# Performance work log

Hardware: AMD Instinct MI355X
Metric: run time of the kernel (lower is better)

The kernel has to match this reference:

```python
import jax, jax.numpy as jnp
import numpy as np

N_NODES = 1024
CHANNELS = [1, 64, 128]
DENSE = [196608, 256]
SAMPLE_NUMBER = 50


def _glorot(key, shape):
    fan_in, fan_out = shape[0], shape[-1]
    s = jnp.sqrt(6.0 / (fan_in + fan_out))
    return jax.random.uniform(key, shape, jnp.float32, -s, s)


def setup_inputs() -> dict:
    key = jax.random.key(0)
    ks = jax.random.split(key, 20)
    T, B = 16, 64
    inp = {
        "xs_seq": jax.random.normal(ks[0], (T, B, N_NODES, CHANNELS[0]), jnp.float32),
        "adj": jax.random.uniform(ks[1], (N_NODES, N_NODES), jnp.float32) / N_NODES,
    }
    # GCGRU params per layer: gates z, r, candidate n over concat([x, h])
    ki = 2
    for li in range(len(CHANNELS) - 1):
        cin, cout = CHANNELS[li], CHANNELS[li + 1]
        for g in ("z", "r", "n"):
            inp[f"W{g}{li}"] = _glorot(ks[ki], (cin + cout, cout)); ki += 1
            inp[f"b{g}{li}"] = jnp.zeros((cout,), jnp.float32)
    inp["W_mu"] = _glorot(ks[ki], (DENSE[0], DENSE[1])); ki += 1
    inp["b_mu"] = jnp.zeros((DENSE[1],), jnp.float32)
    inp["W_lv"] = _glorot(ks[ki], (DENSE[0], DENSE[1])); ki += 1
    inp["b_lv"] = jnp.zeros((DENSE[1],), jnp.float32)
    return inp


def _gcgru(xs, adj, Wz, bz, Wr, br, Wn, bn, cout):
    # xs: [T, B, N, cin]; graph-conv GRU over time via scan
    T, B, N, _ = xs.shape
    h0 = jnp.zeros((B, N, cout), xs.dtype)

    def gconv(a, x, W, b):  # adj @ x @ W + b
        return jnp.einsum("ij,bjc,cd->bid", a, x, W) + b

    def step(h, x):
        xh = jnp.concatenate([x, h], axis=-1)
        z = jax.nn.sigmoid(gconv(adj, xh, Wz, bz))
        r = jax.nn.sigmoid(gconv(adj, xh, Wr, br))
        xrh = jnp.concatenate([x, r * h], axis=-1)
        n = jnp.tanh(gconv(adj, xrh, Wn, bn))
        h_new = (1.0 - z) * h + z * n
        return h_new, h_new

    _, hs = jax.lax.scan(step, h0, xs)
    return hs  # [T, B, N, cout]


def _forward(xs_seq, adj, Wz0, bz0, Wr0, br0, Wn0, bn0,
             Wz1, bz1, Wr1, br1, Wn1, bn1, W_mu, b_mu, W_lv, b_lv, eps):
    h1 = _gcgru(xs_seq, adj, Wz0, bz0, Wr0, br0, Wn0, bn0, CHANNELS[1])
    h2 = _gcgru(h1, adj, Wz1, bz1, Wr1, br1, Wn1, bn1, CHANNELS[2])
    xs = jnp.concatenate([h1[-1], h2[-1]], axis=2)  # [B, N, C1+C2]
    B = xs.shape[0]
    xs = xs.reshape(B, -1)  # [B, N*(C1+C2)]
    mu = jax.nn.sigmoid(xs @ W_mu + b_mu)
    logvar = jax.nn.sigmoid(xs @ W_lv + b_lv)
    std = jnp.exp(0.5 * logvar)
    z = mu + eps * std
    return z, mu, logvar


def reference(xs_seq, adj, Wz0, bz0, Wr0, br0, Wn0, bn0,
              Wz1, bz1, Wr1, br1, Wn1, bn1, W_mu, b_mu, W_lv, b_lv):
    B = xs_seq.shape[1]
    ekey = jax.random.fold_in(jax.random.key(0), 1234)
    eps = jax.random.normal(ekey, (SAMPLE_NUMBER, B, DENSE[1]), jnp.float32).mean(0)
    return _forward(xs_seq, adj, Wz0, bz0, Wr0, br0, Wn0, bn0,
                    Wz1, bz1, Wr1, br1, Wn1, bn1, W_mu, b_mu, W_lv, b_lv, eps)
```

## Files before the change

### kernel.cpp

```cpp
#include <hip/hip_runtime.h>
#include <math.h>

#define EPS_MODE 0

typedef unsigned short u16;
typedef short bf16x8 __attribute__((ext_vector_type(8)));
typedef float f32x4 __attribute__((ext_vector_type(4)));
typedef u16 u16x4 __attribute__((ext_vector_type(4)));
typedef u16 u16x8 __attribute__((ext_vector_type(8)));

static constexpr int T = 16;
static constexpr size_t MF = 1u << 20;
static constexpr int DKCH = 256;
static constexpr int DKCHUNK = 196608 / DKCH;

__device__ __forceinline__ u16 f2bf(float f) {
  unsigned u = __float_as_uint(f);
  unsigned r = (u + 0x7fffu + ((u >> 16) & 1u)) >> 16;
  return (u16)r;
}
__device__ __forceinline__ float bf2f(u16 h) {
  return __uint_as_float(((unsigned)h) << 16);
}
__device__ __forceinline__ void gload16(const void* g, void* l) {
  __builtin_amdgcn_global_load_lds(
      (const __attribute__((address_space(1))) void*)g,
      (__attribute__((address_space(3))) void*)l, 16, 0, 0);
}

__global__ __launch_bounds__(256) void cast_bf16(const float* __restrict__ in,
                                                 u16* __restrict__ out, int n) {
  int i = (blockIdx.x * 256 + threadIdx.x) * 4;
  if (i < n) {
    float4 v = *reinterpret_cast<const float4*>(&in[i]);
    out[i + 0] = f2bf(v.x); out[i + 1] = f2bf(v.y);
    out[i + 2] = f2bf(v.z); out[i + 3] = f2bf(v.w);
  }
}

__global__ __launch_bounds__(256) void prep_wt(const float* __restrict__ Wz0, const float* __restrict__ Wr0,
                                               const float* __restrict__ Wn0, const float* __restrict__ Wz1,
                                               const float* __restrict__ Wr1, const float* __restrict__ Wn1,
                                               u16* __restrict__ WzrT0, u16* __restrict__ WnT0,
                                               u16* __restrict__ WzrT1, u16* __restrict__ WnT1) {
  int seg = blockIdx.y;
  int idx = blockIdx.x * 256 + threadIdx.x;
  if (seg == 0) {
    if (idx < 128 * 64) {
      int j = idx >> 6, k = idx & 63;
      float v = (j < 64) ? Wz0[(k + 1) * 64 + j] : Wr0[(k + 1) * 64 + (j - 64)];
      WzrT0[idx] = f2bf(v);
    }
  } else if (seg == 1) {
    if (idx < 64 * 64) {
      int j = idx >> 6, k = idx & 63;
      WnT0[idx] = f2bf(Wn0[(k + 1) * 64 + j]);
    }
  } else if (seg == 2) {
    if (idx < 256 * 192) {
      int j = idx / 192, k = idx % 192;
      float v = (j < 128) ? Wz1[k * 128 + j] : Wr1[k * 128 + (j - 128)];
      WzrT1[idx] = f2bf(v);
    }
  } else {
    if (idx < 128 * 192) {
      int j = idx / 192, k = idx % 192;
      WnT1[idx] = f2bf(Wn1[k * 128 + j]);
    }
  }
}

template <int EPI, int LOGC, int MFR>
__device__ __forceinline__ void dev_adj_mfma(int bx, int by, char* lds,
                                             const u16* __restrict__ A,
                                             const u16* __restrict__ BT,
                                             void* __restrict__ OUT) {
  constexpr int MT = MFR * 32;
  int tid = threadIdx.x;
  int w = tid >> 6, lane = tid & 63;
  int row0 = by * MT, col0 = bx * 128;
  int wm = w >> 1, wn = w & 1;
  f32x4 acc[MFR][4] = {};
  for (int k0 = 0; k0 < 1024; k0 += 64) {
#pragma unroll
    for (int q = 0; q < MFR; ++q) {
      int row = q * 32 + w * 8 + (lane >> 3);
      gload16(A + (size_t)(row0 + row) * 1024 + k0 + (lane & 7) * 8,
              lds + q * 4096 + w * 1024);
    }
#pragma unroll
    for (int q = 0; q < 4; ++q) {
      int row = q * 32 + w * 8 + (lane >> 3);
      gload16(BT + (size_t)(col0 + row) * 1024 + k0 + (lane & 7) * 8,
              lds + MFR * 4096 + q * 4096 + w * 1024);
    }
    __syncthreads();
#pragma unroll
    for (int kk = 0; kk < 2; ++kk) {
      bf16x8 a[MFR], bb[4];
#pragma unroll
      for (int m = 0; m < MFR; ++m)
        a[m] = *(const bf16x8*)(lds + (wm * (MFR * 16) + m * 16 + (lane & 15)) * 128 + kk * 64 + (lane >> 4) * 16);
#pragma unroll
      for (int n = 0; n < 4; ++n)
        bb[n] = *(const bf16x8*)(lds + MFR * 4096 + (wn * 64 + n * 16 + (lane & 15)) * 128 + kk * 64 + (lane >> 4) * 16);
#pragma unroll
      for (int m = 0; m < MFR; ++m)
#pragma unroll
        for (int n = 0; n < 4; ++n)
          acc[m][n] = __builtin_amdgcn_mfma_f32_16x16x32_bf16(a[m], bb[n], acc[m][n], 0, 0, 0);
    }
    __syncthreads();
  }
  if (EPI == 1) {
    float* O = (float*)OUT;
#pragma unroll
    for (int m = 0; m < MFR; ++m)
#pragma unroll
      for (int n = 0; n < 4; ++n) {
        int col = col0 + wn * 64 + n * 16 + (lane & 15);
        int t = col >> 6, bbx = col & 63;
        int row = row0 + wm * (MFR * 16) + m * 16 + ((lane >> 4) << 2);
        *(float4*)&O[((size_t)t << 16) + ((size_t)bbx << 10) + row] = *(float4*)&acc[m][n];
      }
  } else {
    u16* O = (u16*)OUT;
    constexpr int C = 1 << LOGC;
#pragma unroll
    for (int m = 0; m < MFR; ++m)
#pragma unroll
      for (int n = 0; n < 4; ++n) {
        int col = col0 + wn * 64 + n * 16 + (lane & 15);
        int bbx = col >> LOGC, c = col & (C - 1);
#pragma unroll
        for (int j = 0; j < 4; ++j) {
          int row = row0 + wm * (MFR * 16) + m * 16 + ((lane >> 4) << 2) + j;
          O[(((size_t)bbx << 10) + row) * C + c] = f2bf(acc[m][n][j]);
        }
      }
  }
}

template <int EPI, int LOGC, int MFR>
__global__ __launch_bounds__(256) void adj_mfma(const u16* __restrict__ A,
                                                const u16* __restrict__ BT,
                                                void* __restrict__ OUT) {
  __shared__ __align__(16) char lds[(MFR + 4) * 4096];
  dev_adj_mfma<EPI, LOGC, MFR>(blockIdx.x, blockIdx.y, lds, A, BT, OUT);
}

template <int C, int RK1, int MFR>
__device__ __forceinline__ void dev_adj_ngate(
    int bx, int by, char* lds,
    const u16* __restrict__ A, const u16* __restrict__ BT,
    const u16* __restrict__ WnT, const float* __restrict__ bias,
    const float* __restrict__ axv, const float* __restrict__ wx,
    const u16* __restrict__ AH1, const u16* __restrict__ zT,
    u16* __restrict__ hT) {
  constexpr int LOGC = (C == 64) ? 6 : 7;
  constexpr int KW = (C == 64) ? 64 : 192;
  constexpr int KKAN = C / 32;
  constexpr int MT = MFR * 32;
  int tid = threadIdx.x;
  int w = tid >> 6, lane = tid & 63;
  int row0 = by * MT, col0 = bx * 128;
  int wm = w >> 1, wn = w & 1;
  f32x4 acc[MFR][4] = {};
  for (int k0 = 0; k0 < 1024; k0 += 64) {
#pragma unroll
    for (int q = 0; q < MFR; ++q) {
      int row = q * 32 + w * 8 + (lane >> 3);
      gload16(A + (size_t)(row0 + row) * 1024 + k0 + (lane & 7) * 8,
              lds + q * 4096 + w * 1024);
    }
#pragma unroll
    for (int q = 0; q < 4; ++q) {
      int row = q * 32 + w * 8 + (lane >> 3);
      gload16(BT + (size_t)(col0 + row) * 1024 + k0 + (lane & 7) * 8,
              lds + MFR * 4096 + q * 4096 + w * 1024);
    }
    __syncthreads();
#pragma unroll
    for (int kk = 0; kk < 2; ++kk) {
      bf16x8 a[MFR], bb[4];
#pragma unroll
      for (int m = 0; m < MFR; ++m)
        a[m] = *(const bf16x8*)(lds + (wm * (MFR * 16) + m * 16 + (lane & 15)) * 128 + kk * 64 + (lane >> 4) * 16);
#pragma unroll
      for (int n = 0; n < 4; ++n)
        bb[n] = *(const bf16x8*)(lds + MFR * 4096 + (wn * 64 + n * 16 + (lane & 15)) * 128 + kk * 64 + (lane >> 4) * 16);
#pragma unroll
      for (int m = 0; m < MFR; ++m)
#pragma unroll
        for (int n = 0; n < 4; ++n)
          acc[m][n] = __builtin_amdgcn_mfma_f32_16x16x32_bf16(a[m], bb[n], acc[m][n], 0, 0, 0);
    }
    __syncthreads();
  }
  u16* ANt = (u16*)lds;
#pragma unroll
  for (int m = 0; m < MFR; ++m)
#pragma unroll
    for (int n = 0; n < 4; ++n) {
      int cl = wn * 64 + n * 16 + (lane & 15);
      int rl = wm * (MFR * 16) + m * 16 + ((lane >> 4) << 2);
#pragma unroll
      for (int j = 0; j < 4; ++j)
        ANt[(rl + j) * 136 + cl] = f2bf(acc[m][n][j]);
    }
  __syncthreads();
  int wrow = w >> 1, half = w & 1;
  int arow0 = wrow * (MFR * 16);
  int b0 = col0 >> LOGC;
  int out0 = (C == 64) ? 0 : half * 64;
  int kbase = (C == 64) ? half * 64 : 0;
  int b_eff = (C == 64) ? (b0 + half) : b0;
  constexpr int WOFF = (C == 64) ? 0 : 64;
  f32x4 acc2[MFR][4] = {};
#pragma unroll
  for (int kk = 0; kk < KKAN; ++kk) {
    bf16x8 a[MFR], bb[4];
    int ka = kbase + kk * 32 + (lane >> 4) * 8;
#pragma unroll
    for (int m = 0; m < MFR; ++m)
      a[m] = *(const bf16x8*)&ANt[(arow0 + m * 16 + (lane & 15)) * 136 + ka];
#pragma unroll
    for (int n = 0; n < 4; ++n)
      bb[n] = *(const bf16x8*)&WnT[(size_t)(out0 + n * 16 + (lane & 15)) * KW + WOFF + kk * 32 + (lane >> 4) * 8];
#pragma unroll
    for (int m = 0; m < MFR; ++m)
#pragma unroll
      for (int n = 0; n < 4; ++n)
        acc2[m][n] = __builtin_amdgcn_mfma_f32_16x16x32_bf16(a[m], bb[n], acc2[m][n], 0, 0, 0);
  }
  if (C == 128) {
#pragma unroll
    for (int kk = 0; kk < 2; ++kk) {
      bf16x8 a[MFR], bb[4];
#pragma unroll
      for (int m = 0; m < MFR; ++m)
        a[m] = *(const bf16x8*)&AH1[(((size_t)b0 << 10) + row0 + arow0 + m * 16 + (lane & 15)) * 64 + kk * 32 + (lane >> 4) * 8];
#pragma unroll
      for (int n = 0; n < 4; ++n)
        bb[n] = *(const bf16x8*)&WnT[(size_t)(out0 + n * 16 + (lane & 15)) * 192 + kk * 32 + (lane >> 4) * 8];
#pragma unroll
      for (int m = 0; m < MFR; ++m)
#pragma unroll
        for (int n = 0; n < 4; ++n)
          acc2[m][n] = __builtin_amdgcn_mfma_f32_16x16x32_bf16(a[m], bb[n], acc2[m][n], 0, 0, 0);
    }
  }
#pragma unroll
  for (int m = 0; m < MFR; ++m) {
    float ax4[4];
    if (RK1) {
      float4 v = *(const float4*)&axv[((size_t)b_eff << 10) + row0 + arow0 + m * 16 + ((lane >> 4) << 2)];
      ax4[0] = v.x; ax4[1] = v.y; ax4[2] = v.z; ax4[3] = v.w;
    }
#pragma unroll
    for (int n = 0; n < 4; ++n) {
      int cp = out0 + n * 16 + (lane & 15);
      int grow = arow0 + m * 16 + ((lane >> 4) << 2);
      size_t idx = (((size_t)b_eff << LOGC) + cp) * 1024 + row0 + grow;
      u16x4 zv = *(const u16x4*)&zT[idx];
      u16x4 hv = *(const u16x4*)&hT[idx];
      u16x4 pk;
#pragma unroll
      for (int j = 0; j < 4; ++j) {
        float g = acc2[m][n][j] + bias[cp];
        if (RK1) g += ax4[j] * wx[cp];
        float nv = tanhf(g);
        float z = bf2f(zv[j]), ho = bf2f(hv[j]);
        pk[j] = f2bf((1.f - z) * ho + z * nv);
      }
      *(u16x4*)&hT[idx] = pk;
    }
  }
}

template <int C, int RK1, int MFR>
__global__ __launch_bounds__(256) void adj_ngate(
    const u16* __restrict__ A, const u16* __restrict__ BT,
    const u16* __restrict__ WnT, const float* __restrict__ bias,
    const float* __restrict__ axv, const float* __restrict__ wx,
    const u16* __restrict__ AH1, const u16* __restrict__ zT,
    u16* __restrict__ hT) {
  constexpr int MT = MFR * 32;
  constexpr int STG = (MFR + 4) * 4096;
  constexpr int ANB = MT * 136 * 2;
  constexpr int LDSZ = STG > ANB ? STG : ANB;
  __shared__ __align__(16) char lds[LDSZ];
  dev_adj_ngate<C, RK1, MFR>(blockIdx.x, blockIdx.y, lds, A, BT, WnT, bias, axv, wx,
                             AH1, zT, hT);
}

template <int WM, int WN, int C, int NK1, int NK, int RK1>
__device__ __forceinline__ void dev_gate_zr(
    int by, char* lds,
    const u16* __restrict__ A1, const u16* __restrict__ A2,
    const u16* __restrict__ WT, const float* __restrict__ bz,
    const float* __restrict__ br, const float* __restrict__ axv,
    const float* __restrict__ wxz, const float* __restrict__ wxr,
    const u16* __restrict__ hT, u16* __restrict__ zTo, u16* __restrict__ rhTo) {
  constexpr int MT = WM * 64, NT = WN * 64, K = NK * 64;
  constexpr int NB = 1024 / MT;
  int tid = threadIdx.x;
  int w = tid >> 6, lane = tid & 63;
  int b = by / NB, n0 = (by % NB) * MT;
  size_t row0 = ((size_t)b << 10) + n0;
  int wm = w / WN, wn = w % WN;
  f32x4 acc[4][4] = {};
  for (int s = 0; s < NK; ++s) {
    const u16* As; int astr, koff;
    if (s < NK1) { As = A1; astr = 64; koff = s * 64; }
    else         { As = A2; astr = 128; koff = (s - NK1) * 64; }
#pragma unroll
    for (int q = 0; q < MT / 32; ++q) {
      int row = q * 32 + w * 8 + (lane >> 3);
      gload16(As + (row0 + row) * astr + koff + (lane & 7) * 8,
              lds + q * 4096 + w * 1024);
    }
#pragma unroll
    for (int q = 0; q < NT / 32; ++q) {
      int row = q * 32 + w * 8 + (lane >> 3);
      gload16(WT + (size_t)row * K + s * 64 + (lane & 7) * 8,
              lds + MT * 128 + q * 4096 + w * 1024);
    }
    __syncthreads();
#pragma unroll
    for (int kk = 0; kk < 2; ++kk) {
      bf16x8 a[4], bb[4];
#pragma unroll
      for (int m = 0; m < 4; ++m)
        a[m] = *(const bf16x8*)(lds + (wm * 64 + m * 16 + (lane & 15)) * 128 + kk * 64 + (lane >> 4) * 16);
#pragma unroll
      for (int n = 0; n < 4; ++n)
        bb[n] = *(const bf16x8*)(lds + MT * 128 + (wn * 64 + n * 16 + (lane & 15)) * 128 + kk * 64 + (lane >> 4) * 16);
#pragma unroll
      for (int m = 0; m < 4; ++m)
#pragma unroll
        for (int n = 0; n < 4; ++n)
          acc[m][n] = __builtin_amdgcn_mfma_f32_16x16x32_bf16(a[m], bb[n], acc[m][n], 0, 0, 0);
    }
    __syncthreads();
  }
#pragma unroll
  for (int m = 0; m < 4; ++m) {
    float ax4[4];
    if (RK1) {
      float4 v = *(const float4*)&axv[row0 + wm * 64 + m * 16 + ((lane >> 4) << 2)];
      ax4[0] = v.x; ax4[1] = v.y; ax4[2] = v.z; ax4[3] = v.w;
    }
#pragma unroll
    for (int n = 0; n < 4; ++n) {
      int cp = wn * 64 + n * 16 + (lane & 15);
      bool iz = cp < C;
      int c = iz ? cp : cp - C;
      int rl = wm * 64 + m * 16 + ((lane >> 4) << 2);
      size_t idx = (((size_t)b * C + c) << 10) + n0 + rl;
      u16x4 hv;
      if (!iz) hv = *(const u16x4*)&hT[idx];
      u16x4 pk;
#pragma unroll
      for (int j = 0; j < 4; ++j) {
        float g = acc[m][n][j] + (iz ? bz : br)[c];
        if (RK1) g += ax4[j] * (iz ? wxz : wxr)[c];
        float sg = 1.f / (1.f + expf(-g));
        pk[j] = iz ? f2bf(sg) : f2bf(sg * bf2f(hv[j]));
      }
      *(u16x4*)&(iz ? zTo : rhTo)[idx] = pk;
    }
  }
}

template <int WM, int WN, int C, int NK1, int NK, int RK1>
__global__ __launch_bounds__(256) void gate_zr(
    const u16* __restrict__ A1, const u16* __restrict__ A2,
    const u16* __restrict__ WT, const float* __restrict__ bz,
    const float* __restrict__ br, const float* __restrict__ axv,
    const float* __restrict__ wxz, const float* __restrict__ wxr,
    const u16* __restrict__ hT, u16* __restrict__ zTo, u16* __restrict__ rhTo) {
  __shared__ __align__(16) char lds[WM * 64 * 128 + WN * 64 * 128];
  dev_gate_zr<WM, WN, C, NK1, NK, RK1>(blockIdx.x, lds, A1, A2, WT, bz, br, axv,
                                       wxz, wxr, hT, zTo, rhTo);
}

__global__ __launch_bounds__(256) void combo_zr(
    const u16* __restrict__ AH1, const u16* __restrict__ AH2,
    const u16* __restrict__ WzrT1, const float* __restrict__ bz1, const float* __restrict__ br1,
    const u16* __restrict__ h2T, u16* __restrict__ z1T, u16* __restrict__ rh1T,
    const u16* __restrict__ WzrT0, const float* __restrict__ bz0, const float* __restrict__ br0,
    const float* __restrict__ AXt1, const float* __restrict__ Wz0, const float* __restrict__ Wr0,
    const u16* __restrict__ h1T, u16* __restrict__ z0T, u16* __restrict__ rh0T) {
  __shared__ __align__(16) char lds[40960];
  int bid = blockIdx.x;
  if (bid < 1024)
    dev_gate_zr<1, 4, 128, 1, 3, 0>(bid, lds, AH1, AH2, WzrT1, bz1, br1, nullptr,
                                    nullptr, nullptr, h2T, z1T, rh1T);
  else
    dev_gate_zr<2, 2, 64, 1, 1, 1>(bid - 1024, lds, AH1, nullptr, WzrT0, bz0, br0,
                                   AXt1, Wz0, Wr0, h1T, z0T, rh0T);
}

__global__ __launch_bounds__(256) void combo_ngate(
    const u16* __restrict__ adjB,
    const u16* __restrict__ rh1T, const u16* __restrict__ WnT1, const float* __restrict__ bn1,
    const u16* __restrict__ AH1, const u16* __restrict__ z1T, u16* __restrict__ h2T,
    const u16* __restrict__ rh0T, const u16* __restrict__ WnT0, const float* __restrict__ bn0,
    const float* __restrict__ AXt1, const float* __restrict__ Wn0,
    const u16* __restrict__ z0T, u16* __restrict__ h1T) {
  __shared__ __align__(16) char lds[34816];
  int bid = blockIdx.x;
  if (bid < 512)
    dev_adj_ngate<128, 0, 4>(bid & 63, bid >> 6, lds, adjB, rh1T, WnT1, bn1,
                             nullptr, nullptr, AH1, z1T, h2T);
  else {
    int b2 = bid - 512;
    dev_adj_ngate<64, 1, 4>(b2 & 31, b2 >> 5, lds, adjB, rh0T, WnT0, bn0,
                            AXt1, Wn0, nullptr, z0T, h1T);
  }
}

__global__ __launch_bounds__(256) void combo_ah(
    const u16* __restrict__ adjB, const u16* __restrict__ h2T, u16* __restrict__ AH2,
    const u16* __restrict__ h1T, u16* __restrict__ AH1) {
  __shared__ __align__(16) char lds[32768];
  int bid = blockIdx.x;
  if (bid < 512)
    dev_adj_mfma<0, 7, 4>(bid & 63, bid >> 6, lds, adjB, h2T, AH2);
  else {
    int b2 = bid - 512;
    dev_adj_mfma<0, 6, 4>(b2 & 31, b2 >> 5, lds, adjB, h1T, AH1);
  }
}

__global__ __launch_bounds__(256) void transpose_x(const u16* __restrict__ h1T,
                                                   const u16* __restrict__ h2T,
                                                   u16* __restrict__ X) {
  int b = blockIdx.x;
  int n0 = blockIdx.y * 128;
  __shared__ u16 tile[192][136];
  int tid = threadIdx.x;
#pragma unroll
  for (int i = 0; i < 12; ++i) {
    int id = tid + i * 256;
    int c = id >> 4, g = id & 15;
    u16x8 v;
    if (c < 64) v = *(const u16x8*)&h1T[(((size_t)b << 6) + c) * 1024 + n0 + g * 8];
    else        v = *(const u16x8*)&h2T[(((size_t)b << 7) + (c - 64)) * 1024 + n0 + g * 8];
    *(u16x8*)&tile[c][g * 8] = v;
  }
  __syncthreads();
#pragma unroll
  for (int i = 0; i < 12; ++i) {
    int id = tid + i * 256;
    int n = id / 24, g = id % 24;
    u16x8 v;
#pragma unroll
    for (int j = 0; j < 8; ++j) v[j] = tile[g * 8 + j][n];
    *(u16x8*)&X[(size_t)b * 196608 + (size_t)(n0 + n) * 192 + g * 8] = v;
  }
}

__global__ __launch_bounds__(256) void dense_split(const u16* __restrict__ X,
                                                   const float* __restrict__ Wmu,
                                                   const float* __restrict__ Wlv,
                                                   float* __restrict__ P) {
  int ot = blockIdx.x, ch = blockIdx.y, mat = blockIdx.z;
  const float* W = mat ? Wlv : Wmu;
  int o0 = ot * 64;
  __shared__ float As[16][68];
  __shared__ float Ws[16][68];
  int tid = threadIdx.x;
  int tx = tid & 15, ty = tid >> 4;
  int ab = tid >> 2, akq = (tid & 3) * 4;
  int wkk = tid >> 4, wo4 = (tid & 15) * 4;
  int kb = ch * DKCHUNK;
  float acc[4][4] = {};
  u16x4 xa = *(const u16x4*)&X[(size_t)ab * 196608 + kb + akq];
  float4 wv = *(const float4*)&W[(size_t)(kb + wkk) * 256 + o0 + wo4];
  for (int s = 0; s < DKCHUNK / 16; ++s) {
#pragma unroll
    for (int j = 0; j < 4; ++j) As[akq + j][ab] = bf2f(xa[j]);
    *(float4*)&Ws[wkk][wo4] = wv;
    __syncthreads();
    if (s + 1 < DKCHUNK / 16) {
      int k0 = kb + (s + 1) * 16;
      xa = *(const u16x4*)&X[(size_t)ab * 196608 + k0 + akq];
      wv = *(const float4*)&W[(size_t)(k0 + wkk) * 256 + o0 + wo4];
    }
#pragma unroll
    for (int kk = 0; kk < 16; ++kk) {
      float a[4], bq[4];
      *(float4*)a = *(const float4*)&As[kk][ty * 4];
      *(float4*)bq = *(const float4*)&Ws[kk][tx * 4];
#pragma unroll
      for (int i = 0; i < 4; ++i)
#pragma unroll
        for (int j = 0; j < 4; ++j) acc[i][j] += a[i] * bq[j];
    }
    __syncthreads();
  }
#pragma unroll
  for (int i = 0; i < 4; ++i) {
    float4 v; v.x = acc[i][0]; v.y = acc[i][1]; v.z = acc[i][2]; v.w = acc[i][3];
    *(float4*)&P[(((size_t)mat * DKCH + ch) * 64 + ty * 4 + i) * 256 + o0 + tx * 4] = v;
  }
}

__device__ __forceinline__ unsigned rotl32(unsigned v, int s) {
  return (v << s) | (v >> (32 - s));
}
__device__ void threefry(unsigned k0, unsigned k1, unsigned x0, unsigned x1,
                         unsigned& o0, unsigned& o1) {
  unsigned ks2 = k0 ^ k1 ^ 0x1BD11BDAu;
  unsigned a = x0 + k0, b = x1 + k1;
#define TF_RND(rot) { a += b; b = rotl32(b, rot); b ^= a; }
  TF_RND(13) TF_RND(15) TF_RND(26) TF_RND(6)
  a += k1; b += ks2 + 1u;
  TF_RND(17) TF_RND(29) TF_RND(16) TF_RND(24)
  a += ks2; b += k0 + 2u;
  TF_RND(13) TF_RND(15) TF_RND(26) TF_RND(6)
  a += k0; b += k1 + 3u;
  TF_RND(17) TF_RND(29) TF_RND(16) TF_RND(24)
  a += k1; b += ks2 + 4u;
  TF_RND(13) TF_RND(15) TF_RND(26) TF_RND(6)
  a += ks2; b += k0 + 5u;
#undef TF_RND
  o0 = a; o1 = b;
}

__device__ float u32_to_normal(unsigned bits) {
  unsigned fb = (bits >> 9) | 0x3F800000u;
  float f = __uint_as_float(fb) - 1.0f;
  const float lo = -0.99999994f;
  float u = f * 2.0f + lo;
  u = fmaxf(lo, u);
  float w = -log1pf(-u * u);
  float p;
  if (w < 5.0f) {
    w -= 2.5f;
    p = 2.81022636e-08f;
    p = fmaf(p, w, 3.43273939e-07f);
    p = fmaf(p, w, -3.5233877e-06f);
    p = fmaf(p, w, -4.39150654e-06f);
    p = fmaf(p, w, 0.00021858087f);
    p = fmaf(p, w, -0.00125372503f);
    p = fmaf(p, w, -0.00417768164f);
    p = fmaf(p, w, 0.246640727f);
    p = fmaf(p, w, 1.50140941f);
  } else {
    w = sqrtf(w) - 3.0f;
    p = -0.000200214257f;
    p = fmaf(p, w, 0.000100950558f);
    p = fmaf(p, w, 0.00134934322f);
    p = fmaf(p, w, -0.00367342844f);
    p = fmaf(p, w, 0.00573950773f);
    p = fmaf(p, w, -0.0076224613f);
    p = fmaf(p, w, 0.00943887047f);
    p = fmaf(p, w, 1.00167406f);
    p = fmaf(p, w, 2.83297682f);
  }
  return 1.41421354f * (p * u);
}

__global__ __launch_bounds__(256) void eps_kernel(float* __restrict__ eps) {
  int b = blockIdx.x;
  int o = threadIdx.x;
  unsigned k0, k1;
  threefry(0u, 0u, 0u, 1234u, k0, k1);
  float s = 0.f;
  for (int smp = 0; smp < 50; ++smp) {
    unsigned idx = ((unsigned)smp * 64u + (unsigned)b) * 256u + (unsigned)o;
    unsigned o0, o1, bits;
#if EPS_MODE == 0
    threefry(k0, k1, 0u, idx, o0, o1);
    bits = o0 ^ o1;
#else
    unsigned pp = idx % 409600u, half = idx / 409600u;
    threefry(k0, k1, pp, pp + 409600u, o0, o1);
    bits = half ? o1 : o0;
#endif
    s += u32_to_normal(bits);
  }
  eps[b * 256 + o] = s / 50.0f;
}

__global__ __launch_bounds__(256) void final_kernel(const float* __restrict__ P,
                                                    const float* __restrict__ bmu,
                                                    const float* __restrict__ blv,
                                                    const float* __restrict__ eps,
                                                    float* __restrict__ out) {
  int b = blockIdx.x, o = threadIdx.x;
  float smu = 0.f, slv = 0.f;
  for (int ch = 0; ch < DKCH; ++ch) {
    smu += P[(((size_t)0 * DKCH + ch) * 64 + b) * 256 + o];
    slv += P[(((size_t)1 * DKCH + ch) * 64 + b) * 256 + o];
  }
  float mu = 1.f / (1.f + expf(-(smu + bmu[o])));
  float lv = 1.f / (1.f + expf(-(slv + blv[o])));
  float z = mu + eps[b * 256 + o] * expf(0.5f * lv);
  out[b * 256 + o] = z;
  out[16384 + b * 256 + o] = mu;
  out[32768 + b * 256 + o] = lv;
}

extern "C" void kernel_launch(void* const* d_in, const int* in_sizes, int n_in,
                              void* d_out, int out_size, void* d_ws, size_t ws_size,
                              hipStream_t stream) {
  (void)in_sizes; (void)n_in; (void)out_size; (void)ws_size;
  const float* xs  = (const float*)d_in[0];
  const float* adj = (const float*)d_in[1];
  const float* Wz0 = (const float*)d_in[2];  const float* bz0 = (const float*)d_in[3];
  const float* Wr0 = (const float*)d_in[4];  const float* br0 = (const float*)d_in[5];
  const float* Wn0 = (const float*)d_in[6];  const float* bn0 = (const float*)d_in[7];
  const float* Wz1 = (const float*)d_in[8];  const float* bz1 = (const float*)d_in[9];
  const float* Wr1 = (const float*)d_in[10]; const float* br1 = (const float*)d_in[11];
  const float* Wn1 = (const float*)d_in[12]; const float* bn1 = (const float*)d_in[13];
  const float* Wmu = (const float*)d_in[14]; const float* bmu = (const float*)d_in[15];
  const float* Wlv = (const float*)d_in[16]; const float* blv = (const float*)d_in[17];

  float* ws = (float*)d_ws;
  u16*  adjB  = (u16*)(ws);
  u16*  xsB   = (u16*)(ws + MF / 2);
  float* AXv  = ws + 1 * MF;
  u16*  h1T   = (u16*)(ws + 2 * MF);
  u16*  h2T   = (u16*)(ws + 4 * MF);
  u16*  z0T   = (u16*)(ws + 8 * MF);
  u16*  z1T   = (u16*)(ws + 10 * MF);
  u16*  rh0T  = (u16*)(ws + 14 * MF);
  u16*  rh1T  = (u16*)(ws + 16 * MF);
  u16*  AH1   = (u16*)(ws + 20 * MF);
  u16*  AH2   = (u16*)(ws + 22 * MF);
  u16*  WTb   = (u16*)(ws + 26 * MF);
  u16*  X     = (u16*)(ws + 8 * MF);
  float* P    = ws + 16 * MF;
  float* EPS  = ws + 24 * MF;

  u16* WzrT0 = WTb;
  u16* WnT0  = WTb + 8192;
  u16* WzrT1 = WTb + 12288;
  u16* WnT1  = WTb + 61440;

  hipMemsetAsync(ws + 2 * MF, 0, 6 * MF * sizeof(float), stream);
  hipMemsetAsync(ws + 20 * MF, 0, 6 * MF * sizeof(float), stream);

  cast_bf16<<<1024, 256, 0, stream>>>(adj, adjB, 1 << 20);
  cast_bf16<<<1024, 256, 0, stream>>>(xs, xsB, 1 << 20);
  prep_wt<<<dim3(192, 4), 256, 0, stream>>>(Wz0, Wr0, Wn0, Wz1, Wr1, Wn1,
                                            WzrT0, WnT0, WzrT1, WnT1);

  adj_mfma<1, 0, 4><<<dim3(8, 8), 256, 0, stream>>>(adjB, xsB, AXv);

  gate_zr<2, 2, 64, 1, 1, 1><<<512, 256, 0, stream>>>(
      AH1, nullptr, WzrT0, bz0, br0, AXv, Wz0, Wr0, h1T, z0T, rh0T);
  adj_ngate<64, 1, 4><<<dim3(32, 8), 256, 0, stream>>>(
      adjB, rh0T, WnT0, bn0, AXv, Wn0, nullptr, z0T, h1T);
  adj_mfma<0, 6, 4><<<dim3(32, 8), 256, 0, stream>>>(adjB, h1T, AH1);

  for (int i = 0; i < T - 1; ++i) {
    const float* AXt1 = AXv + (size_t)(i + 1) * 65536;
    combo_zr<<<1536, 256, 0, stream>>>(AH1, AH2, WzrT1, bz1, br1, h2T, z1T, rh1T,
                                       WzrT0, bz0, br0, AXt1, Wz0, Wr0, h1T, z0T, rh0T);
    combo_ngate<<<768, 256, 0, stream>>>(adjB, rh1T, WnT1, bn1, AH1, z1T, h2T,
                                         rh0T, WnT0, bn0, AXt1, Wn0, z0T, h1T);
    combo_ah<<<768, 256, 0, stream>>>(adjB, h2T, AH2, h1T, AH1);
  }

  gate_zr<1, 4, 128, 1, 3, 0><<<1024, 256, 0, stream>>>(
      AH1, AH2, WzrT1, bz1, br1, nullptr, nullptr, nullptr, h2T, z1T, rh1T);
  adj_ngate<128, 0, 4><<<dim3(64, 8), 256, 0, stream>>>(
      adjB, rh1T, WnT1, bn1, nullptr, nullptr, AH1, z1T, h2T);

  transpose_x<<<dim3(64, 8), 256, 0, stream>>>(h1T, h2T, X);
  dense_split<<<dim3(4, DKCH, 2), 256, 0, stream>>>(X, Wmu, Wlv, P);
  eps_kernel<<<64, 256, 0, stream>>>(EPS);
  final_kernel<<<64, 256, 0, stream>>>(P, bmu, blv, EPS, (float*)d_out);
}
```

Measured before the change: 3.125 ms.

## Fuse adjacency aggregation with z/r gates per step and use MFMA for dense head

Each recurrent step now runs one kernel that computes adj·[h1,h2] for a 128-row panel and keeps the result in LDS. From that tile it applies the layer-1 z/r gate GEMMs and the next step's layer-0 z/r gates, so combo_zr, combo_ah and the AH2 buffer go away. This cuts one launch per step and a global round trip of the aggregated features, at the cost of fewer blocks (512) and heavier per-block work. The final dense layer also switches from a scalar FP32 tiled GEMM to bf16 MFMA by truncating the FP32 weights in LDS, which adds precision risk.

```diff
diff --git a/kernel.cpp b/kernel.cpp
--- a/kernel.cpp
+++ b/kernel.cpp
@@ -27,6 +27,7 @@
       (const __attribute__((address_space(1))) void*)g,
       (__attribute__((address_space(3))) void*)l, 16, 0, 0);
 }
+__device__ __forceinline__ float sigm(float x) { return 1.f / (1.f + expf(-x)); }
 
 __global__ __launch_bounds__(256) void cast_bf16(const float* __restrict__ in,
                                                  u16* __restrict__ out, int n) {
@@ -294,114 +295,6 @@
                              AH1, zT, hT);
 }
 
-template <int WM, int WN, int C, int NK1, int NK, int RK1>
-__device__ __forceinline__ void dev_gate_zr(
-    int by, char* lds,
-    const u16* __restrict__ A1, const u16* __restrict__ A2,
-    const u16* __restrict__ WT, const float* __restrict__ bz,
-    const float* __restrict__ br, const float* __restrict__ axv,
-    const float* __restrict__ wxz, const float* __restrict__ wxr,
-    const u16* __restrict__ hT, u16* __restrict__ zTo, u16* __restrict__ rhTo) {
-  constexpr int MT = WM * 64, NT = WN * 64, K = NK * 64;
-  constexpr int NB = 1024 / MT;
-  int tid = threadIdx.x;
-  int w = tid >> 6, lane = tid & 63;
-  int b = by / NB, n0 = (by % NB) * MT;
-  size_t row0 = ((size_t)b << 10) + n0;
-  int wm = w / WN, wn = w % WN;
-  f32x4 acc[4][4] = {};
-  for (int s = 0; s < NK; ++s) {
-    const u16* As; int astr, koff;
-    if (s < NK1) { As = A1; astr = 64; koff = s * 64; }
-    else         { As = A2; astr = 128; koff = (s - NK1) * 64; }
-#pragma unroll
-    for (int q = 0; q < MT / 32; ++q) {
-      int row = q * 32 + w * 8 + (lane >> 3);
-      gload16(As + (row0 + row) * astr + koff + (lane & 7) * 8,
-              lds + q * 4096 + w * 1024);
-    }
-#pragma unroll
-    for (int q = 0; q < NT / 32; ++q) {
-      int row = q * 32 + w * 8 + (lane >> 3);
-      gload16(WT + (size_t)row * K + s * 64 + (lane & 7) * 8,
-              lds + MT * 128 + q * 4096 + w * 1024);
-    }
-    __syncthreads();
-#pragma unroll
-    for (int kk = 0; kk < 2; ++kk) {
-      bf16x8 a[4], bb[4];
-#pragma unroll
-      for (int m = 0; m < 4; ++m)
-        a[m] = *(const bf16x8*)(lds + (wm * 64 + m * 16 + (lane & 15)) * 128 + kk * 64 + (lane >> 4) * 16);
-#pragma unroll
-      for (int n = 0; n < 4; ++n)
-        bb[n] = *(const bf16x8*)(lds + MT * 128 + (wn * 64 + n * 16 + (lane & 15)) * 128 + kk * 64 + (lane >> 4) * 16);
-#pragma unroll
-      for (int m = 0; m < 4; ++m)
-#pragma unroll
-        for (int n = 0; n < 4; ++n)
-          acc[m][n] = __builtin_amdgcn_mfma_f32_16x16x32_bf16(a[m], bb[n], acc[m][n], 0, 0, 0);
-    }
-    __syncthreads();
-  }
-#pragma unroll
-  for (int m = 0; m < 4; ++m) {
-    float ax4[4];
-    if (RK1) {
-      float4 v = *(const float4*)&axv[row0 + wm * 64 + m * 16 + ((lane >> 4) << 2)];
-      ax4[0] = v.x; ax4[1] = v.y; ax4[2] = v.z; ax4[3] = v.w;
-    }
-#pragma unroll
-    for (int n = 0; n < 4; ++n) {
-      int cp = wn * 64 + n * 16 + (lane & 15);
-      bool iz = cp < C;
-      int c = iz ? cp : cp - C;
-      int rl = wm * 64 + m * 16 + ((lane >> 4) << 2);
-      size_t idx = (((size_t)b * C + c) << 10) + n0 + rl;
-      u16x4 hv;
-      if (!iz) hv = *(const u16x4*)&hT[idx];
-      u16x4 pk;
-#pragma unroll
-      for (int j = 0; j < 4; ++j) {
-        float g = acc[m][n][j] + (iz ? bz : br)[c];
-        if (RK1) g += ax4[j] * (iz ? wxz : wxr)[c];
-        float sg = 1.f / (1.f + expf(-g));
-        pk[j] = iz ? f2bf(sg) : f2bf(sg * bf2f(hv[j]));
-      }
-      *(u16x4*)&(iz ? zTo : rhTo)[idx] = pk;
-    }
-  }
-}
-
-template <int WM, int WN, int C, int NK1, int NK, int RK1>
-__global__ __launch_bounds__(256) void gate_zr(
-    const u16* __restrict__ A1, const u16* __restrict__ A2,
-    const u16* __restrict__ WT, const float* __restrict__ bz,
-    const float* __restrict__ br, const float* __restrict__ axv,
-    const float* __restrict__ wxz, const float* __restrict__ wxr,
-    const u16* __restrict__ hT, u16* __restrict__ zTo, u16* __restrict__ rhTo) {
-  __shared__ __align__(16) char lds[WM * 64 * 128 + WN * 64 * 128];
-  dev_gate_zr<WM, WN, C, NK1, NK, RK1>(blockIdx.x, lds, A1, A2, WT, bz, br, axv,
-                                       wxz, wxr, hT, zTo, rhTo);
-}
-
-__global__ __launch_bounds__(256) void combo_zr(
-    const u16* __restrict__ AH1, const u16* __restrict__ AH2,
-    const u16* __restrict__ WzrT1, const float* __restrict__ bz1, const float* __restrict__ br1,
-    const u16* __restrict__ h2T, u16* __restrict__ z1T, u16* __restrict__ rh1T,
-    const u16* __restrict__ WzrT0, const float* __restrict__ bz0, const float* __restrict__ br0,
-    const float* __restrict__ AXt1, const float* __restrict__ Wz0, const float* __restrict__ Wr0,
-    const u16* __restrict__ h1T, u16* __restrict__ z0T, u16* __restrict__ rh0T) {
-  __shared__ __align__(16) char lds[40960];
-  int bid = blockIdx.x;
-  if (bid < 1024)
-    dev_gate_zr<1, 4, 128, 1, 3, 0>(bid, lds, AH1, AH2, WzrT1, bz1, br1, nullptr,
-                                    nullptr, nullptr, h2T, z1T, rh1T);
-  else
-    dev_gate_zr<2, 2, 64, 1, 1, 1>(bid - 1024, lds, AH1, nullptr, WzrT0, bz0, br0,
-                                   AXt1, Wz0, Wr0, h1T, z0T, rh0T);
-}
-
 __global__ __launch_bounds__(256) void combo_ngate(
     const u16* __restrict__ adjB,
     const u16* __restrict__ rh1T, const u16* __restrict__ WnT1, const float* __restrict__ bn1,
@@ -421,16 +314,233 @@
   }
 }
 
-__global__ __launch_bounds__(256) void combo_ah(
-    const u16* __restrict__ adjB, const u16* __restrict__ h2T, u16* __restrict__ AH2,
-    const u16* __restrict__ h1T, u16* __restrict__ AH1) {
-  __shared__ __align__(16) char lds[32768];
-  int bid = blockIdx.x;
-  if (bid < 512)
-    dev_adj_mfma<0, 7, 4>(bid & 63, bid >> 6, lds, adjB, h2T, AH2);
-  else {
-    int b2 = bid - 512;
-    dev_adj_mfma<0, 6, 4>(b2 & 31, b2 >> 5, lds, adjB, h1T, AH1);
+template <int WM, int WN, int C, int NK1, int NK, int RK1>
+__global__ __launch_bounds__(256) void gate_zr(
+    const u16* __restrict__ A1, const u16* __restrict__ A2,
+    const u16* __restrict__ WT, const float* __restrict__ bz,
+    const float* __restrict__ br, const float* __restrict__ axv,
+    const float* __restrict__ wxz, const float* __restrict__ wxr,
+    const u16* __restrict__ hT, u16* __restrict__ zTo, u16* __restrict__ rhTo) {
+  constexpr int MT = WM * 64, NT = WN * 64, K = NK * 64;
+  constexpr int NB = 1024 / MT;
+  __shared__ __align__(16) char lds[MT * 128 + NT * 128];
+  int tid = threadIdx.x;
+  int w = tid >> 6, lane = tid & 63;
+  int by = blockIdx.x;
+  int b = by / NB, n0 = (by % NB) * MT;
+  size_t row0 = ((size_t)b << 10) + n0;
+  int wm = w / WN, wn = w % WN;
+  f32x4 acc[4][4] = {};
+  for (int s = 0; s < NK; ++s) {
+    const u16* As; int astr, koff;
+    if (s < NK1) { As = A1; astr = 64; koff = s * 64; }
+    else         { As = A2; astr = 128; koff = (s - NK1) * 64; }
+#pragma unroll
+    for (int q = 0; q < MT / 32; ++q) {
+      int row = q * 32 + w * 8 + (lane >> 3);
+      gload16(As + (row0 + row) * astr + koff + (lane & 7) * 8,
+              lds + q * 4096 + w * 1024);
+    }
+#pragma unroll
+    for (int q = 0; q < NT / 32; ++q) {
+      int row = q * 32 + w * 8 + (lane >> 3);
+      gload16(WT + (size_t)row * K + s * 64 + (lane & 7) * 8,
+              lds + MT * 128 + q * 4096 + w * 1024);
+    }
+    __syncthreads();
+#pragma unroll
+    for (int kk = 0; kk < 2; ++kk) {
+      bf16x8 a[4], bb[4];
+#pragma unroll
+      for (int m = 0; m < 4; ++m)
+        a[m] = *(const bf16x8*)(lds + (wm * 64 + m * 16 + (lane & 15)) * 128 + kk * 64 + (lane >> 4) * 16);
+#pragma unroll
+      for (int n = 0; n < 4; ++n)
+        bb[n] = *(const bf16x8*)(lds + MT * 128 + (wn * 64 + n * 16 + (lane & 15)) * 128 + kk * 64 + (lane >> 4) * 16);
+#pragma unroll
+      for (int m = 0; m < 4; ++m)
+#pragma unroll
+        for (int n = 0; n < 4; ++n)
+          acc[m][n] = __builtin_amdgcn_mfma_f32_16x16x32_bf16(a[m], bb[n], acc[m][n], 0, 0, 0);
+    }
+    __syncthreads();
+  }
+#pragma unroll
+  for (int m = 0; m < 4; ++m) {
+    float ax4[4];
+    if (RK1) {
+      float4 v = *(const float4*)&axv[row0 + wm * 64 + m * 16 + ((lane >> 4) << 2)];
+      ax4[0] = v.x; ax4[1] = v.y; ax4[2] = v.z; ax4[3] = v.w;
+    }
+#pragma unroll
+    for (int n = 0; n < 4; ++n) {
+      int cp = wn * 64 + n * 16 + (lane & 15);
+      bool iz = cp < C;
+      int c = iz ? cp : cp - C;
+      int rl = wm * 64 + m * 16 + ((lane >> 4) << 2);
+      size_t idx = (((size_t)b * C + c) << 10) + n0 + rl;
+      u16x4 hv;
+      if (!iz) hv = *(const u16x4*)&hT[idx];
+      u16x4 pk;
+#pragma unroll
+      for (int j = 0; j < 4; ++j) {
+        float g = acc[m][n][j] + (iz ? bz : br)[c];
+        if (RK1) g += ax4[j] * (iz ? wxz : wxr)[c];
+        float sg = sigm(g);
+        pk[j] = iz ? f2bf(sg) : f2bf(sg * bf2f(hv[j]));
+      }
+      *(u16x4*)&(iz ? zTo : rhTo)[idx] = pk;
+    }
+  }
+}
+
+__global__ __launch_bounds__(256) void fused_F(
+    const u16* __restrict__ adjB, const u16* __restrict__ h1T, const u16* __restrict__ h2T,
+    const u16* __restrict__ WzrT1, const float* __restrict__ bz1, const float* __restrict__ br1,
+    const u16* __restrict__ WzrT0, const float* __restrict__ bz0, const float* __restrict__ br0,
+    const float* __restrict__ AXt2, const float* __restrict__ wz0x, const float* __restrict__ wr0x,
+    u16* __restrict__ AH1, u16* __restrict__ z1T, u16* __restrict__ rh1T,
+    u16* __restrict__ z0T, u16* __restrict__ rh0T, int do_zr0) {
+  __shared__ __align__(16) char lds[51200];
+  int tid = threadIdx.x, w = tid >> 6, lane = tid & 63;
+  int b = blockIdx.x >> 3, panel = blockIdx.x & 7;
+  int row0 = panel * 128;
+  int wm = w >> 1, wn = w & 1;
+  f32x4 acc[4][6] = {};
+  for (int k0 = 0; k0 < 1024; k0 += 64) {
+#pragma unroll
+    for (int q = 0; q < 4; ++q) {
+      int row = q * 32 + w * 8 + (lane >> 3);
+      gload16(adjB + (size_t)(row0 + row) * 1024 + k0 + (lane & 7) * 8,
+              lds + q * 4096 + w * 1024);
+    }
+#pragma unroll
+    for (int q = 0; q < 6; ++q) {
+      int row = q * 32 + w * 8 + (lane >> 3);
+      const u16* src = (q < 2) ? (h1T + (((size_t)b * 64 + row) << 10))
+                               : (h2T + (((size_t)b * 128 + (row - 64)) << 10));
+      gload16(src + k0 + (lane & 7) * 8, lds + 16384 + q * 4096 + w * 1024);
+    }
+    __syncthreads();
+#pragma unroll
+    for (int kk = 0; kk < 2; ++kk) {
+      bf16x8 a[4], bb[6];
+#pragma unroll
+      for (int m = 0; m < 4; ++m)
+        a[m] = *(const bf16x8*)(lds + (wm * 64 + m * 16 + (lane & 15)) * 128 + kk * 64 + (lane >> 4) * 16);
+#pragma unroll
+      for (int n = 0; n < 6; ++n)
+        bb[n] = *(const bf16x8*)(lds + 16384 + (wn * 96 + n * 16 + (lane & 15)) * 128 + kk * 64 + (lane >> 4) * 16);
+#pragma unroll
+      for (int m = 0; m < 4; ++m)
+#pragma unroll
+        for (int n = 0; n < 6; ++n)
+          acc[m][n] = __builtin_amdgcn_mfma_f32_16x16x32_bf16(a[m], bb[n], acc[m][n], 0, 0, 0);
+    }
+    __syncthreads();
+  }
+  u16* AN = (u16*)lds;
+#pragma unroll
+  for (int m = 0; m < 4; ++m)
+#pragma unroll
+    for (int n = 0; n < 6; ++n) {
+      int cl = wn * 96 + n * 16 + (lane & 15);
+      int rl = wm * 64 + m * 16 + ((lane >> 4) << 2);
+#pragma unroll
+      for (int j = 0; j < 4; ++j)
+        AN[(rl + j) * 200 + cl] = f2bf(acc[m][n][j]);
+    }
+  __syncthreads();
+#pragma unroll
+  for (int it = 0; it < 4; ++it) {
+    int id = tid + it * 256;
+    int row = id >> 3, g = id & 7;
+    u16x8 v = *(const u16x8*)&AN[row * 200 + g * 8];
+    *(u16x8*)&AH1[(((size_t)b << 10) + row0 + row) * 64 + g * 8] = v;
+  }
+#pragma unroll
+  for (int hz = 0; hz < 2; ++hz) {
+    f32x4 g1[4][4] = {};
+#pragma unroll
+    for (int kk = 0; kk < 6; ++kk) {
+      bf16x8 a[4], bb[4];
+#pragma unroll
+      for (int m = 0; m < 4; ++m)
+        a[m] = *(const bf16x8*)&AN[(wm * 64 + m * 16 + (lane & 15)) * 200 + kk * 32 + (lane >> 4) * 8];
+#pragma unroll
+      for (int n = 0; n < 4; ++n) {
+        int out = hz * 128 + wn * 64 + n * 16 + (lane & 15);
+        bb[n] = *(const bf16x8*)&WzrT1[(size_t)out * 192 + kk * 32 + (lane >> 4) * 8];
+      }
+#pragma unroll
+      for (int m = 0; m < 4; ++m)
+#pragma unroll
+        for (int n = 0; n < 4; ++n)
+          g1[m][n] = __builtin_amdgcn_mfma_f32_16x16x32_bf16(a[m], bb[n], g1[m][n], 0, 0, 0);
+    }
+#pragma unroll
+    for (int m = 0; m < 4; ++m)
+#pragma unroll
+      for (int n = 0; n < 4; ++n) {
+        int c = wn * 64 + n * 16 + (lane & 15);
+        int grow = wm * 64 + m * 16 + ((lane >> 4) << 2);
+        size_t idx = (((size_t)b * 128 + c) << 10) + row0 + grow;
+        u16x4 pk;
+        if (hz == 0) {
+#pragma unroll
+          for (int j = 0; j < 4; ++j) pk[j] = f2bf(sigm(g1[m][n][j] + bz1[c]));
+          *(u16x4*)&z1T[idx] = pk;
+        } else {
+          u16x4 hv = *(const u16x4*)&h2T[idx];
+#pragma unroll
+          for (int j = 0; j < 4; ++j)
+            pk[j] = f2bf(sigm(g1[m][n][j] + br1[c]) * bf2f(hv[j]));
+          *(u16x4*)&rh1T[idx] = pk;
+        }
+      }
+  }
+  if (do_zr0) {
+    f32x4 g0[4][4] = {};
+#pragma unroll
+    for (int kk = 0; kk < 2; ++kk) {
+      bf16x8 a[4], bb[4];
+#pragma unroll
+      for (int m = 0; m < 4; ++m)
+        a[m] = *(const bf16x8*)&AN[(wm * 64 + m * 16 + (lane & 15)) * 200 + kk * 32 + (lane >> 4) * 8];
+#pragma unroll
+      for (int n = 0; n < 4; ++n) {
+        int out = wn * 64 + n * 16 + (lane & 15);
+        bb[n] = *(const bf16x8*)&WzrT0[(size_t)out * 64 + kk * 32 + (lane >> 4) * 8];
+      }
+#pragma unroll
+      for (int m = 0; m < 4; ++m)
+#pragma unroll
+        for (int n = 0; n < 4; ++n)
+          g0[m][n] = __builtin_amdgcn_mfma_f32_16x16x32_bf16(a[m], bb[n], g0[m][n], 0, 0, 0);
+    }
+#pragma unroll
+    for (int m = 0; m < 4; ++m) {
+      int grow0 = wm * 64 + m * 16 + ((lane >> 4) << 2);
+      float4 axv = *(const float4*)&AXt2[((size_t)b << 10) + row0 + grow0];
+      float ax4[4] = {axv.x, axv.y, axv.z, axv.w};
+#pragma unroll
+      for (int n = 0; n < 4; ++n) {
+        int out = wn * 64 + n * 16 + (lane & 15);
+        bool iz = out < 64;
+        int c = iz ? out : out - 64;
+        size_t idx = (((size_t)b * 64 + c) << 10) + row0 + grow0;
+        u16x4 hv;
+        if (!iz) hv = *(const u16x4*)&h1T[idx];
+        u16x4 pk;
+#pragma unroll
+        for (int j = 0; j < 4; ++j) {
+          float g = g0[m][n][j] + (iz ? bz0 : br0)[c] + ax4[j] * (iz ? wz0x : wr0x)[c];
+          float sg = sigm(g);
+          pk[j] = iz ? f2bf(sg) : f2bf(sg * bf2f(hv[j]));
+        }
+        *(u16x4*)&(iz ? z0T : rh0T)[idx] = pk;
+      }
+    }
   }
 }
 
@@ -462,49 +572,68 @@
   }
 }
 
-__global__ __launch_bounds__(256) void dense_split(const u16* __restrict__ X,
-                                                   const float* __restrict__ Wmu,
-                                                   const float* __restrict__ Wlv,
-                                                   float* __restrict__ P) {
-  int ot = blockIdx.x, ch = blockIdx.y, mat = blockIdx.z;
-  const float* W = mat ? Wlv : Wmu;
-  int o0 = ot * 64;
-  __shared__ float As[16][68];
-  __shared__ float Ws[16][68];
-  int tid = threadIdx.x;
-  int tx = tid & 15, ty = tid >> 4;
-  int ab = tid >> 2, akq = (tid & 3) * 4;
-  int wkk = tid >> 4, wo4 = (tid & 15) * 4;
+__global__ __launch_bounds__(256) void dense_mfma(const u16* __restrict__ X,
+                                                  const float* __restrict__ Wmu,
+                                                  const float* __restrict__ Wlv,
+                                                  float* __restrict__ P) {
+  __shared__ __align__(16) char lds[33280 + 5120];
+  float* Ws = (float*)lds;
+  u16* Xs = (u16*)(lds + 33280);
+  int tid = threadIdx.x, w = tid >> 6, lane = tid & 63;
+  int ch = blockIdx.x, mat = blockIdx.y;
+  const float* Wp = mat ? Wlv : Wmu;
   int kb = ch * DKCHUNK;
-  float acc[4][4] = {};
-  u16x4 xa = *(const u16x4*)&X[(size_t)ab * 196608 + kb + akq];
-  float4 wv = *(const float4*)&W[(size_t)(kb + wkk) * 256 + o0 + wo4];
-  for (int s = 0; s < DKCHUNK / 16; ++s) {
-#pragma unroll
-    for (int j = 0; j < 4; ++j) As[akq + j][ab] = bf2f(xa[j]);
-    *(float4*)&Ws[wkk][wo4] = wv;
-    __syncthreads();
-    if (s + 1 < DKCHUNK / 16) {
-      int k0 = kb + (s + 1) * 16;
-      xa = *(const u16x4*)&X[(size_t)ab * 196608 + k0 + akq];
-      wv = *(const float4*)&W[(size_t)(k0 + wkk) * 256 + o0 + wo4];
-    }
-#pragma unroll
-    for (int kk = 0; kk < 16; ++kk) {
-      float a[4], bq[4];
-      *(float4*)a = *(const float4*)&As[kk][ty * 4];
-      *(float4*)bq = *(const float4*)&Ws[kk][tx * 4];
-#pragma unroll
-      for (int i = 0; i < 4; ++i)
-#pragma unroll
-        for (int j = 0; j < 4; ++j) acc[i][j] += a[i] * bq[j];
-    }
-    __syncthreads();
-  }
-#pragma unroll
-  for (int i = 0; i < 4; ++i) {
-    float4 v; v.x = acc[i][0]; v.y = acc[i][1]; v.z = acc[i][2]; v.w = acc[i][3];
-    *(float4*)&P[(((size_t)mat * DKCH + ch) * 64 + ty * 4 + i) * 256 + o0 + tx * 4] = v;
+  int o4 = (tid & 63) * 4, kk0 = tid >> 6;
+  int xrow = tid >> 2, xg = tid & 3;
+  f32x4 acc[16] = {};
+  float4 wreg[8];
+  u16x8 xreg;
+  {
+    const float* wb = Wp + (size_t)kb * 256;
+#pragma unroll
+    for (int p = 0; p < 8; ++p)
+      wreg[p] = *(const float4*)&wb[(size_t)(kk0 + p * 4) * 256 + o4];
+    xreg = *(const u16x8*)&X[(size_t)xrow * 196608 + kb + xg * 8];
+  }
+  for (int s = 0; s < DKCHUNK / 32; ++s) {
+#pragma unroll
+    for (int p = 0; p < 8; ++p)
+      *(float4*)&Ws[(kk0 + p * 4) * 260 + o4] = wreg[p];
+    *(u16x8*)&Xs[xrow * 40 + xg * 8] = xreg;
+    __syncthreads();
+    if (s + 1 < DKCHUNK / 32) {
+      int k1 = kb + (s + 1) * 32;
+      const float* wb = Wp + (size_t)k1 * 256;
+#pragma unroll
+      for (int p = 0; p < 8; ++p)
+        wreg[p] = *(const float4*)&wb[(size_t)(kk0 + p * 4) * 256 + o4];
+      xreg = *(const u16x8*)&X[(size_t)xrow * 196608 + k1 + xg * 8];
+    }
+    bf16x8 af = *(const bf16x8*)&Xs[(w * 16 + (lane & 15)) * 40 + (lane >> 4) * 8];
+    int kq = (lane >> 4) * 8;
+#pragma unroll
+    for (int n = 0; n < 16; ++n) {
+      int o = n * 16 + (lane & 15);
+      unsigned rr[4];
+#pragma unroll
+      for (int j = 0; j < 4; ++j) {
+        unsigned lo = *(const u16*)((const char*)&Ws[(kq + 2 * j) * 260 + o] + 2);
+        unsigned hi = *(const u16*)((const char*)&Ws[(kq + 2 * j + 1) * 260 + o] + 2);
+        rr[j] = lo | (hi << 16);
+      }
+      bf16x8 bv = *(const bf16x8*)rr;
+      acc[n] = __builtin_amdgcn_mfma_f32_16x16x32_bf16(af, bv, acc[n], 0, 0, 0);
+    }
+    __syncthreads();
+  }
+#pragma unroll
+  for (int n = 0; n < 16; ++n) {
+    int o = n * 16 + (lane & 15);
+#pragma unroll
+    for (int j = 0; j < 4; ++j) {
+      int brow = w * 16 + ((lane >> 4) << 2) + j;
+      P[(((size_t)mat * DKCH + ch) * 64 + brow) * 256 + o] = acc[n][j];
+    }
   }
 }
 
@@ -597,8 +726,8 @@
     smu += P[(((size_t)0 * DKCH + ch) * 64 + b) * 256 + o];
     slv += P[(((size_t)1 * DKCH + ch) * 64 + b) * 256 + o];
   }
-  float mu = 1.f / (1.f + expf(-(smu + bmu[o])));
-  float lv = 1.f / (1.f + expf(-(slv + blv[o])));
+  float mu = sigm(smu + bmu[o]);
+  float lv = sigm(slv + blv[o]);
   float z = mu + eps[b * 256 + o] * expf(0.5f * lv);
   out[b * 256 + o] = z;
   out[16384 + b * 256 + o] = mu;
@@ -631,11 +760,10 @@
   u16*  rh0T  = (u16*)(ws + 14 * MF);
   u16*  rh1T  = (u16*)(ws + 16 * MF);
   u16*  AH1   = (u16*)(ws + 20 * MF);
-  u16*  AH2   = (u16*)(ws + 22 * MF);
   u16*  WTb   = (u16*)(ws + 26 * MF);
   u16*  X     = (u16*)(ws + 8 * MF);
   float* P    = ws + 16 * MF;
-  float* EPS  = ws + 24 * MF;
+  float* EPS  = ws + 25 * MF;
 
   u16* WzrT0 = WTb;
   u16* WnT0  = WTb + 8192;
@@ -643,7 +771,7 @@
   u16* WnT1  = WTb + 61440;
 
   hipMemsetAsync(ws + 2 * MF, 0, 6 * MF * sizeof(float), stream);
-  hipMemsetAsync(ws + 20 * MF, 0, 6 * MF * sizeof(float), stream);
+  hipMemsetAsync(ws + 20 * MF, 0, 2 * MF * sizeof(float), stream);
 
   cast_bf16<<<1024, 256, 0, stream>>>(adj, adjB, 1 << 20);
   cast_bf16<<<1024, 256, 0, stream>>>(xs, xsB, 1 << 20);
@@ -656,24 +784,23 @@
       AH1, nullptr, WzrT0, bz0, br0, AXv, Wz0, Wr0, h1T, z0T, rh0T);
   adj_ngate<64, 1, 4><<<dim3(32, 8), 256, 0, stream>>>(
       adjB, rh0T, WnT0, bn0, AXv, Wn0, nullptr, z0T, h1T);
-  adj_mfma<0, 6, 4><<<dim3(32, 8), 256, 0, stream>>>(adjB, h1T, AH1);
-
-  for (int i = 0; i < T - 1; ++i) {
-    const float* AXt1 = AXv + (size_t)(i + 1) * 65536;
-    combo_zr<<<1536, 256, 0, stream>>>(AH1, AH2, WzrT1, bz1, br1, h2T, z1T, rh1T,
-                                       WzrT0, bz0, br0, AXt1, Wz0, Wr0, h1T, z0T, rh0T);
-    combo_ngate<<<768, 256, 0, stream>>>(adjB, rh1T, WnT1, bn1, AH1, z1T, h2T,
-                                         rh0T, WnT0, bn0, AXt1, Wn0, z0T, h1T);
-    combo_ah<<<768, 256, 0, stream>>>(adjB, h2T, AH2, h1T, AH1);
-  }
-
-  gate_zr<1, 4, 128, 1, 3, 0><<<1024, 256, 0, stream>>>(
-      AH1, AH2, WzrT1, bz1, br1, nullptr, nullptr, nullptr, h2T, z1T, rh1T);
-  adj_ngate<128, 0, 4><<<dim3(64, 8), 256, 0, stream>>>(
-      adjB, rh1T, WnT1, bn1, nullptr, nullptr, AH1, z1T, h2T);
+
+  for (int i = -1; i <= T - 2; ++i) {
+    int do0 = (i < T - 2) ? 1 : 0;
+    const float* AXt2 = AXv + (size_t)(do0 ? (i + 2) : 0) * 65536;
+    fused_F<<<512, 256, 0, stream>>>(adjB, h1T, h2T, WzrT1, bz1, br1,
+                                     WzrT0, bz0, br0, AXt2, Wz0, Wr0,
+                                     AH1, z1T, rh1T, z0T, rh0T, do0);
+    if (i < T - 2)
+      combo_ngate<<<768, 256, 0, stream>>>(adjB, rh1T, WnT1, bn1, AH1, z1T, h2T,
+                                           rh0T, WnT0, bn0, AXt2, Wn0, z0T, h1T);
+    else
+      adj_ngate<128, 0, 4><<<dim3(64, 8), 256, 0, stream>>>(
+          adjB, rh1T, WnT1, bn1, nullptr, nullptr, AH1, z1T, h2T);
+  }
 
   transpose_x<<<dim3(64, 8), 256, 0, stream>>>(h1T, h2T, X);
-  dense_split<<<dim3(4, DKCH, 2), 256, 0, stream>>>(X, Wmu, Wlv, P);
+  dense_mfma<<<dim3(DKCH, 2), 256, 0, stream>>>(X, Wmu, Wlv, P);
   eps_kernel<<<64, 256, 0, stream>>>(EPS);
   final_kernel<<<64, 256, 0, stream>>>(P, bmu, blv, EPS, (float*)d_out);
 }
```

Measured after the change: 3.353 ms. 7.3% more time.
